# Optimization experiments

Measured on AMD Instinct MI355X. Metric: run time of the kernel, lower is better.

The kernel has to match this reference:

```python
import jax, jax.numpy as jnp
import numpy as np


def setup_inputs() -> dict:
    key = jax.random.key(0)
    k1, k2, k3, k4 = jax.random.split(key, 4)
    B, S, IN, H = 4, 2048, 512, 1024
    x = jax.random.normal(k1, (B, S, IN), dtype=jnp.float32)
    W1 = jax.random.normal(k2, (IN, H), dtype=jnp.float32) * (1.0 / np.sqrt(IN))
    b1 = jax.random.normal(k3, (H,), dtype=jnp.float32) * 0.02
    Wq = jax.random.normal(k4, (H, H), dtype=jnp.float32) * (1.0 / np.sqrt(H))
    return {"x": x, "W1": W1, "b1": b1, "Wq": Wq, "atten_size": 16}


def reference(x, W1, b1, Wq, atten_size):
    A = atten_size
    B, S, _ = x.shape
    H = W1.shape[1]
    h = jax.nn.relu(jnp.einsum('bsi,ih->bsh', x, W1) + b1)  # [B,S,H]
    # zero-pad sequence dim by A on each side
    padded = jnp.pad(h, ((0, 0), (A, A), (0, 0)))  # [B,S+2A,H]
    # torch: stack(roll(padded, k, 1) for k in -A..A, dim=2) then slice [A:-A]
    # => x_nei[b, i, j] = padded[b, 2A + i - j]
    idx = 2 * A + jnp.arange(S)[:, None] - jnp.arange(2 * A + 1)[None, :]  # [S,W]
    x_nei = padded[:, idx, :]  # [B,S,W,H]
    q = jnp.einsum('bsh,hk->bsk', h, Wq)  # [B,S,H]
    scores = jnp.einsum('bsh,bswh->bsw', q, x_nei) / jnp.sqrt(jnp.asarray(H, x.dtype))
    w = jax.nn.softmax(scores, axis=2)  # softmax over window axis
    out = jnp.einsum('bsw,bswh->bsh', w, x_nei)
    return out
```

## Files before the change

### kernel.cpp

```cpp
#include <hip/hip_runtime.h>
#include <stdint.h>

constexpr int BATCH = 4;
constexpr int SEQ   = 2048;
constexpr int DIN   = 512;
constexpr int DH    = 1024;
constexpr int BS    = BATCH * SEQ;
constexpr int AP    = 32;
constexpr int AW    = 64;

typedef float  floatx4 __attribute__((ext_vector_type(4)));
typedef short  bf16x8  __attribute__((ext_vector_type(8)));

static __device__ __forceinline__ unsigned short f2bf(float f) {
  union { float f; unsigned u; } v; v.f = f;
  unsigned r = (v.u + 0x7fffu + ((v.u >> 16) & 1u)) >> 16;
  return (unsigned short)r;
}

static __device__ __forceinline__ void gld_lds16(const unsigned short* g, const short* l) {
  typedef const __attribute__((address_space(1))) void* gvp;
  typedef __attribute__((address_space(3))) void* lvp;
  __builtin_amdgcn_global_load_lds((gvp)(uintptr_t)g, (lvp)(unsigned)(uintptr_t)l, 16, 0, 0);
}

__global__ __launch_bounds__(256) void prep_k(const float* __restrict__ X,
                                              const float* __restrict__ W1,
                                              const float* __restrict__ Wq,
                                              unsigned short* __restrict__ Xb,
                                              unsigned short* __restrict__ w1t,
                                              unsigned short* __restrict__ wqt) {
  __shared__ float t[32][33];
  if (blockIdx.y >= 48) {
    const int t0 = ((blockIdx.y - 48) * 32 + blockIdx.x) * 256 + threadIdx.x;
    const float4 a = ((const float4*)X)[(size_t)t0 * 2];
    const float4 b = ((const float4*)X)[(size_t)t0 * 2 + 1];
    __align__(16) unsigned short o[8];
    o[0] = f2bf(a.x); o[1] = f2bf(a.y); o[2] = f2bf(a.z); o[3] = f2bf(a.w);
    o[4] = f2bf(b.x); o[5] = f2bf(b.y); o[6] = f2bf(b.z); o[7] = f2bf(b.w);
    *(uint4*)(Xb + (size_t)t0 * 8) = *(const uint4*)o;
    return;
  }
  const bool isW1 = blockIdx.y < 16;
  const float* in = isW1 ? W1 : Wq;
  unsigned short* out = isW1 ? w1t : wqt;
  const int R = isW1 ? DIN : DH;
  const int C = DH;
  const int r0 = (isW1 ? blockIdx.y : (blockIdx.y - 16)) * 32;
  const int c0 = blockIdx.x * 32;
  const int tx = threadIdx.x & 31, ty = threadIdx.x >> 5;
  for (int i = ty; i < 32; i += 8) t[i][tx] = in[(size_t)(r0 + i) * C + c0 + tx];
  __syncthreads();
  for (int i = ty; i < 32; i += 8) out[(size_t)(c0 + i) * R + r0 + tx] = f2bf(t[tx][i]);
}

__global__ __launch_bounds__(256) void gemm1_k(const unsigned short* __restrict__ Ab,
                                               const unsigned short* __restrict__ Bt,
                                               const float* __restrict__ bias,
                                               unsigned short* __restrict__ outB,
                                               unsigned short* __restrict__ outBT) {
  const int M = BS, N = DH, K = DIN;
  __shared__ __align__(16) short As0[128 * 32], As1[128 * 32];
  __shared__ __align__(16) short Bs0[128 * 32], Bs1[128 * 32];
  const int tid  = threadIdx.x;
  const int m0   = blockIdx.x * 128, n0 = blockIdx.y * 128;
  const int wv   = tid >> 6, lane = tid & 63;
  const int wm   = (wv >> 1) * 64, wn = (wv & 1) * 64;
  const int l16  = lane & 15, quad = lane >> 4;

  const int ra = lane >> 2, ca = (lane & 3) * 8;
  const unsigned short* gA = Ab + (size_t)(m0 + wv * 32 + ra) * K + ca;
  const unsigned short* gB = Bt + (size_t)(n0 + wv * 32 + ra) * K + ca;
  const short* lA0a = &As0[wv * 1024];
  const short* lA0b = &As0[wv * 1024 + 512];
  const short* lA1a = &As1[wv * 1024];
  const short* lA1b = &As1[wv * 1024 + 512];
  const short* lB0a = &Bs0[wv * 1024];
  const short* lB0b = &Bs0[wv * 1024 + 512];
  const short* lB1a = &Bs1[wv * 1024];
  const short* lB1b = &Bs1[wv * 1024 + 512];

  floatx4 acc[4][4];
  for (int i = 0; i < 4; i++)
    for (int j = 0; j < 4; j++) acc[i][j] = {0.f, 0.f, 0.f, 0.f};

  for (int ks = 0; ks < K / 64; ++ks) {
    __syncthreads();
    gld_lds16(gA, lA0a); gld_lds16(gA + 16 * K, lA0b);
    gld_lds16(gA + 32, lA1a); gld_lds16(gA + 16 * K + 32, lA1b);
    gld_lds16(gB, lB0a); gld_lds16(gB + 16 * K, lB0b);
    gld_lds16(gB + 32, lB1a); gld_lds16(gB + 16 * K + 32, lB1b);
    gA += 64; gB += 64;
    __syncthreads();
    bf16x8 af[4], bfr[4];
    for (int i = 0; i < 4; i++)
      af[i] = *(const bf16x8*)&As0[(wm + i * 16 + l16) * 32 + quad * 8];
    for (int j = 0; j < 4; j++)
      bfr[j] = *(const bf16x8*)&Bs0[(wn + j * 16 + l16) * 32 + quad * 8];
    for (int i = 0; i < 4; i++)
      for (int j = 0; j < 4; j++)
        acc[i][j] = __builtin_amdgcn_mfma_f32_16x16x32_bf16(af[i], bfr[j], acc[i][j], 0, 0, 0);
    for (int i = 0; i < 4; i++)
      af[i] = *(const bf16x8*)&As1[(wm + i * 16 + l16) * 32 + quad * 8];
    for (int j = 0; j < 4; j++)
      bfr[j] = *(const bf16x8*)&Bs1[(wn + j * 16 + l16) * 32 + quad * 8];
    for (int i = 0; i < 4; i++)
      for (int j = 0; j < 4; j++)
        acc[i][j] = __builtin_amdgcn_mfma_f32_16x16x32_bf16(af[i], bfr[j], acc[i][j], 0, 0, 0);
  }

  for (int j = 0; j < 4; j++) {
    const int col = n0 + wn + j * 16 + l16;
    const float bv = bias[col];
    for (int i = 0; i < 4; i++) {
      const int rowb = m0 + wm + i * 16 + quad * 4;
      float v[4];
      for (int r = 0; r < 4; r++) v[r] = fmaxf(acc[i][j][r] + bv, 0.f);
      for (int r = 0; r < 4; r++) outB[(size_t)(rowb + r) * N + col] = f2bf(v[r]);
      ushort4 o4; o4.x = f2bf(v[0]); o4.y = f2bf(v[1]); o4.z = f2bf(v[2]); o4.w = f2bf(v[3]);
      *(ushort4*)(outBT + (size_t)col * M + rowb) = o4;
    }
  }
}

__global__ __launch_bounds__(1024, 4) void attn_fused_k(const unsigned short* __restrict__ hb,
                                                        const unsigned short* __restrict__ hbT,
                                                        const unsigned short* __restrict__ wqt,
                                                        float* __restrict__ out) {
  __shared__ __align__(16) unsigned short Hq[32 * 1024];
  __shared__ float Sf[2][32 * 64];
  __shared__ __align__(16) short Ps[32 * 72];

  const int tid  = threadIdx.x;
  const int wave = tid >> 6, lane = tid & 63;
  const int l16  = lane & 15, quad = lane >> 4;
  const int p0   = blockIdx.x * AP;
  const int s0   = p0 & (SEQ - 1);

  for (int i = tid; i < 32 * 72 / 2; i += 1024) ((unsigned*)Ps)[i] = 0;

  {
    const int r  = tid >> 5;
    const int c0 = (tid & 31) * 32;
    const unsigned short* src = hb + (size_t)(p0 + r) * DH + c0;
    #pragma unroll
    for (int c = 0; c < 4; c++) {
      uint4 v = *(const uint4*)(src + c * 8);
      const int colu = (c0 + c * 8) ^ ((r & 15) << 3);
      *(uint4*)&Hq[r * 1024 + colu] = v;
    }
  }
  __syncthreads();

  floatx4 qa[2][4];
  {
    for (int i = 0; i < 2; i++)
      for (int j = 0; j < 4; j++) qa[i][j] = {0.f, 0.f, 0.f, 0.f};
    const int wcol = wave * 64;
    const unsigned short* gq = wqt + (size_t)(wcol + l16) * DH + quad * 8;
    #pragma unroll 2
    for (int it = 0; it < 32; ++it) {
      const int cb = it * 32 + quad * 8;
      const int sw = cb ^ (l16 << 3);
      bf16x8 a0 = *(const bf16x8*)&Hq[l16 * 1024 + sw];
      bf16x8 a1 = *(const bf16x8*)&Hq[(16 + l16) * 1024 + sw];
      #pragma unroll
      for (int j = 0; j < 4; j++) {
        bf16x8 b = *(const bf16x8*)(gq + (size_t)(j * 16) * DH + it * 32);
        qa[0][j] = __builtin_amdgcn_mfma_f32_16x16x32_bf16(a0, b, qa[0][j], 0, 0, 0);
        qa[1][j] = __builtin_amdgcn_mfma_f32_16x16x32_bf16(a1, b, qa[1][j], 0, 0, 0);
      }
    }
  }
  __syncthreads();

  {
    const int wcol = wave * 64;
    for (int i = 0; i < 2; i++)
      for (int j = 0; j < 4; j++)
        for (int r = 0; r < 4; r++) {
          const int row  = i * 16 + quad * 4 + r;
          const int colu = wcol + j * 16 + l16;
          Hq[row * 1024 + (colu ^ ((row & 15) << 3))] = f2bf(qa[i][j][r]);
        }
  }
  __syncthreads();

  {
    const int kh = wave & 1;
    const int nt = (wave >> 1) & 3;
    const int mt = wave >> 3;
    const int qrow = mt * 16 + l16;
    const int hrow = s0 - 16 + nt * 16 + l16;
    const bool hv = (hrow >= 0) && (hrow < SEQ);
    const unsigned short* hp = hb + (long long)(p0 - 16 + nt * 16 + l16) * DH + kh * 512 + quad * 8;

    floatx4 ac[4] = {{0,0,0,0},{0,0,0,0},{0,0,0,0},{0,0,0,0}};
    const bf16x8 hz = {0,0,0,0,0,0,0,0};
    __builtin_amdgcn_s_setprio(1);
    #pragma unroll
    for (int it = 0; it < 16; ++it) {
      const int cb = kh * 512 + it * 32 + quad * 8;
      bf16x8 qf = *(const bf16x8*)&Hq[qrow * 1024 + (cb ^ (l16 << 3))];
      bf16x8 ha = hz;
      if (hv) ha = *(const bf16x8*)(hp + it * 32);
      ac[it & 3] = __builtin_amdgcn_mfma_f32_16x16x32_bf16(qf, ha, ac[it & 3], 0, 0, 0);
    }
    __builtin_amdgcn_s_setprio(0);
    floatx4 s4;
    for (int r = 0; r < 4; r++)
      s4[r] = (ac[0][r] + ac[1][r]) + (ac[2][r] + ac[3][r]);
    for (int r = 0; r < 4; r++)
      Sf[kh][(mt * 16 + quad * 4 + r) * 64 + nt * 16 + l16] = s4[r] * (1.f / 32.f);
  }
  __syncthreads();

  if (tid < 512) {
    const int row = tid >> 4, k = tid & 15;
    const float v0 = Sf[0][row * 64 + row + k] + Sf[1][row * 64 + row + k];
    const float v1 = Sf[0][row * 64 + row + k + 16] + Sf[1][row * 64 + row + k + 16];
    const float v2 = (k == 0) ? (Sf[0][row * 64 + row + 32] + Sf[1][row * 64 + row + 32]) : -1e30f;
    float mx = fmaxf(v0, fmaxf(v1, v2));
    for (int off = 1; off < 16; off <<= 1) mx = fmaxf(mx, __shfl_xor(mx, off, 64));
    const float e0 = __expf(v0 - mx), e1 = __expf(v1 - mx);
    const float e2 = (k == 0) ? __expf(v2 - mx) : 0.f;
    float sum = e0 + e1 + e2;
    for (int off = 1; off < 16; off <<= 1) sum += __shfl_xor(sum, off, 64);
    const float inv = 1.f / sum;
    Ps[row * 72 + row + k] = f2bf(e0 * inv);
    Ps[row * 72 + row + k + 16] = f2bf(e1 * inv);
    if (k == 0) Ps[row * 72 + row + 32] = f2bf(e2 * inv);
  }
  __syncthreads();

  {
    const bf16x8 pb00 = *(const bf16x8*)&Ps[(l16) * 72 + quad * 8];
    const bf16x8 pb01 = *(const bf16x8*)&Ps[(l16) * 72 + 32 + quad * 8];
    const bf16x8 pb10 = *(const bf16x8*)&Ps[(16 + l16) * 72 + quad * 8];
    const bf16x8 pb11 = *(const bf16x8*)&Ps[(16 + l16) * 72 + 32 + quad * 8];

    int lo = 16 - s0; if (lo < 0) lo = 0;
    int hi = SEQ + 16 - s0; if (hi > AW) hi = AW;
    const bool interior = (lo == 0) && (hi == AW);

    #pragma unroll
    for (int i = 0; i < 4; ++i) {
      const int mt2 = wave * 4 + i;
      const unsigned short* ap = hbT + (size_t)(mt2 * 16 + l16) * BS + (p0 - 16) + quad * 8;
      bf16x8 aa0 = *(const bf16x8*)(ap);
      bf16x8 aa1 = *(const bf16x8*)(ap + 32);
      if (!interior) {
        #pragma unroll
        for (int j = 0; j < 8; j++) {
          const int k = quad * 8 + j;
          if (k < lo || k >= hi) aa0[j] = 0;
          if (k + 32 < lo || k + 32 >= hi) aa1[j] = 0;
        }
      }
      floatx4 o0 = {0.f, 0.f, 0.f, 0.f}, o1 = {0.f, 0.f, 0.f, 0.f};
      __builtin_amdgcn_s_setprio(1);
      o0 = __builtin_amdgcn_mfma_f32_16x16x32_bf16(aa0, pb00, o0, 0, 0, 0);
      o0 = __builtin_amdgcn_mfma_f32_16x16x32_bf16(aa1, pb01, o0, 0, 0, 0);
      o1 = __builtin_amdgcn_mfma_f32_16x16x32_bf16(aa0, pb10, o1, 0, 0, 0);
      o1 = __builtin_amdgcn_mfma_f32_16x16x32_bf16(aa1, pb11, o1, 0, 0, 0);
      __builtin_amdgcn_s_setprio(0);
      float4 s0v; s0v.x = o0[0]; s0v.y = o0[1]; s0v.z = o0[2]; s0v.w = o0[3];
      float4 s1v; s1v.x = o1[0]; s1v.y = o1[1]; s1v.z = o1[2]; s1v.w = o1[3];
      *(float4*)(out + (size_t)(p0 + l16) * DH + mt2 * 16 + quad * 4) = s0v;
      *(float4*)(out + (size_t)(p0 + 16 + l16) * DH + mt2 * 16 + quad * 4) = s1v;
    }
  }
}

extern "C" void kernel_launch(void* const* d_in, const int* in_sizes, int n_in,
                              void* d_out, int out_size, void* d_ws, size_t ws_size,
                              hipStream_t stream) {
  const float* x  = (const float*)d_in[0];
  const float* W1 = (const float*)d_in[1];
  const float* b1 = (const float*)d_in[2];
  const float* Wq = (const float*)d_in[3];

  char* w = (char*)d_ws;
  unsigned short* w1t = (unsigned short*)(w);
  unsigned short* wqt = (unsigned short*)(w + (1ull  << 20));
  unsigned short* hb  = (unsigned short*)(w + (3ull  << 20));
  unsigned short* hbT = (unsigned short*)(w + (19ull << 20));
  unsigned short* xb  = (unsigned short*)(w + (35ull << 20));

  prep_k<<<dim3(32, 112), 256, 0, stream>>>(x, W1, Wq, xb, w1t, wqt);

  gemm1_k<<<dim3(BS / 128, DH / 128), 256, 0, stream>>>(xb, w1t, b1, hb, hbT);

  attn_fused_k<<<BS / AP, 1024, 0, stream>>>(hb, hbT, wqt, (float*)d_out);
}
```

Measured before the change: 186.6 us.

## Merge prep, GEMM and attention into one cooperative persistent kernel

Replaces the three separate launches with a single cooperative kernel of 256 blocks of 1024 threads, separating the phases with grid-wide syncs. The in-attention Q projection becomes a separate grid-wide GEMM that writes q to global memory (reusing the xb buffer), and the GEMM tiles now use 16 waves with 32x32 per-wave tiles. The aim is to remove launch overhead and the redundant per-block Q recomputation. In exchange it adds grid barriers, gives each wave a smaller MFMA tile, and adds an extra global round-trip for q. Aliasing qb onto xb is safe only because xb is no longer read once gemm1 has finished.

```diff
diff --git a/kernel.cpp b/kernel.cpp
--- a/kernel.cpp
+++ b/kernel.cpp
@@ -1,5 +1,8 @@
 #include <hip/hip_runtime.h>
+#include <hip/hip_cooperative_groups.h>
 #include <stdint.h>
+
+namespace cg = cooperative_groups;
 
 constexpr int BATCH = 4;
 constexpr int SEQ   = 2048;
@@ -24,250 +27,215 @@
   __builtin_amdgcn_global_load_lds((gvp)(uintptr_t)g, (lvp)(unsigned)(uintptr_t)l, 16, 0, 0);
 }
 
-__global__ __launch_bounds__(256) void prep_k(const float* __restrict__ X,
-                                              const float* __restrict__ W1,
-                                              const float* __restrict__ Wq,
-                                              unsigned short* __restrict__ Xb,
-                                              unsigned short* __restrict__ w1t,
-                                              unsigned short* __restrict__ wqt) {
-  __shared__ float t[32][33];
-  if (blockIdx.y >= 48) {
-    const int t0 = ((blockIdx.y - 48) * 32 + blockIdx.x) * 256 + threadIdx.x;
-    const float4 a = ((const float4*)X)[(size_t)t0 * 2];
-    const float4 b = ((const float4*)X)[(size_t)t0 * 2 + 1];
-    __align__(16) unsigned short o[8];
-    o[0] = f2bf(a.x); o[1] = f2bf(a.y); o[2] = f2bf(a.z); o[3] = f2bf(a.w);
-    o[4] = f2bf(b.x); o[5] = f2bf(b.y); o[6] = f2bf(b.z); o[7] = f2bf(b.w);
-    *(uint4*)(Xb + (size_t)t0 * 8) = *(const uint4*)o;
-    return;
-  }
-  const bool isW1 = blockIdx.y < 16;
-  const float* in = isW1 ? W1 : Wq;
-  unsigned short* out = isW1 ? w1t : wqt;
-  const int R = isW1 ? DIN : DH;
-  const int C = DH;
-  const int r0 = (isW1 ? blockIdx.y : (blockIdx.y - 16)) * 32;
-  const int c0 = blockIdx.x * 32;
-  const int tx = threadIdx.x & 31, ty = threadIdx.x >> 5;
-  for (int i = ty; i < 32; i += 8) t[i][tx] = in[(size_t)(r0 + i) * C + c0 + tx];
-  __syncthreads();
-  for (int i = ty; i < 32; i += 8) out[(size_t)(c0 + i) * R + r0 + tx] = f2bf(t[tx][i]);
-}
-
-__global__ __launch_bounds__(256) void gemm1_k(const unsigned short* __restrict__ Ab,
-                                               const unsigned short* __restrict__ Bt,
-                                               const float* __restrict__ bias,
-                                               unsigned short* __restrict__ outB,
-                                               unsigned short* __restrict__ outBT) {
-  const int M = BS, N = DH, K = DIN;
-  __shared__ __align__(16) short As0[128 * 32], As1[128 * 32];
-  __shared__ __align__(16) short Bs0[128 * 32], Bs1[128 * 32];
-  const int tid  = threadIdx.x;
-  const int m0   = blockIdx.x * 128, n0 = blockIdx.y * 128;
-  const int wv   = tid >> 6, lane = tid & 63;
-  const int wm   = (wv >> 1) * 64, wn = (wv & 1) * 64;
-  const int l16  = lane & 15, quad = lane >> 4;
-
+static __device__ __forceinline__ void do_gemm(
+    const unsigned short* __restrict__ Ab, const unsigned short* __restrict__ Bt,
+    const float* __restrict__ bias, unsigned short* __restrict__ outB,
+    unsigned short* __restrict__ outBT, int M, int N, int K, int m0, int n0,
+    int tid, char* smemc) {
+  short (*Sm)[128 * 32] = (short (*)[128 * 32])smemc;
+  const int wv = tid >> 6, lane = tid & 63;
+  const int wm = (wv >> 2) * 32, wn = (wv & 3) * 32;
+  const int l16 = lane & 15, quad = lane >> 4;
   const int ra = lane >> 2, ca = (lane & 3) * 8;
-  const unsigned short* gA = Ab + (size_t)(m0 + wv * 32 + ra) * K + ca;
-  const unsigned short* gB = Bt + (size_t)(n0 + wv * 32 + ra) * K + ca;
-  const short* lA0a = &As0[wv * 1024];
-  const short* lA0b = &As0[wv * 1024 + 512];
-  const short* lA1a = &As1[wv * 1024];
-  const short* lA1b = &As1[wv * 1024 + 512];
-  const short* lB0a = &Bs0[wv * 1024];
-  const short* lB0b = &Bs0[wv * 1024 + 512];
-  const short* lB1a = &Bs1[wv * 1024];
-  const short* lB1b = &Bs1[wv * 1024 + 512];
-
-  floatx4 acc[4][4];
-  for (int i = 0; i < 4; i++)
-    for (int j = 0; j < 4; j++) acc[i][j] = {0.f, 0.f, 0.f, 0.f};
+  const int wA = wv & 7;
+  const bool isB = wv >= 8;
+  const unsigned short* gS =
+      (isB ? Bt + (size_t)(n0 + wA * 16 + ra) * K : Ab + (size_t)(m0 + wA * 16 + ra) * K) + ca;
+  const short* l0 = &Sm[isB ? 2 : 0][wA * 512];
+  const short* l1 = &Sm[isB ? 3 : 1][wA * 512];
+
+  floatx4 acc[2][2];
+  for (int i = 0; i < 2; i++)
+    for (int j = 0; j < 2; j++) acc[i][j] = {0.f, 0.f, 0.f, 0.f};
 
   for (int ks = 0; ks < K / 64; ++ks) {
     __syncthreads();
-    gld_lds16(gA, lA0a); gld_lds16(gA + 16 * K, lA0b);
-    gld_lds16(gA + 32, lA1a); gld_lds16(gA + 16 * K + 32, lA1b);
-    gld_lds16(gB, lB0a); gld_lds16(gB + 16 * K, lB0b);
-    gld_lds16(gB + 32, lB1a); gld_lds16(gB + 16 * K + 32, lB1b);
-    gA += 64; gB += 64;
-    __syncthreads();
-    bf16x8 af[4], bfr[4];
-    for (int i = 0; i < 4; i++)
-      af[i] = *(const bf16x8*)&As0[(wm + i * 16 + l16) * 32 + quad * 8];
-    for (int j = 0; j < 4; j++)
-      bfr[j] = *(const bf16x8*)&Bs0[(wn + j * 16 + l16) * 32 + quad * 8];
-    for (int i = 0; i < 4; i++)
-      for (int j = 0; j < 4; j++)
-        acc[i][j] = __builtin_amdgcn_mfma_f32_16x16x32_bf16(af[i], bfr[j], acc[i][j], 0, 0, 0);
-    for (int i = 0; i < 4; i++)
-      af[i] = *(const bf16x8*)&As1[(wm + i * 16 + l16) * 32 + quad * 8];
-    for (int j = 0; j < 4; j++)
-      bfr[j] = *(const bf16x8*)&Bs1[(wn + j * 16 + l16) * 32 + quad * 8];
-    for (int i = 0; i < 4; i++)
-      for (int j = 0; j < 4; j++)
-        acc[i][j] = __builtin_amdgcn_mfma_f32_16x16x32_bf16(af[i], bfr[j], acc[i][j], 0, 0, 0);
-  }
-
-  for (int j = 0; j < 4; j++) {
+    gld_lds16(gS, l0);
+    gld_lds16(gS + 32, l1);
+    gS += 64;
+    __syncthreads();
+    bf16x8 a0 = *(const bf16x8*)&Sm[0][(wm + l16) * 32 + quad * 8];
+    bf16x8 a1 = *(const bf16x8*)&Sm[0][(wm + 16 + l16) * 32 + quad * 8];
+    bf16x8 b0 = *(const bf16x8*)&Sm[2][(wn + l16) * 32 + quad * 8];
+    bf16x8 b1 = *(const bf16x8*)&Sm[2][(wn + 16 + l16) * 32 + quad * 8];
+    acc[0][0] = __builtin_amdgcn_mfma_f32_16x16x32_bf16(a0, b0, acc[0][0], 0, 0, 0);
+    acc[0][1] = __builtin_amdgcn_mfma_f32_16x16x32_bf16(a0, b1, acc[0][1], 0, 0, 0);
+    acc[1][0] = __builtin_amdgcn_mfma_f32_16x16x32_bf16(a1, b0, acc[1][0], 0, 0, 0);
+    acc[1][1] = __builtin_amdgcn_mfma_f32_16x16x32_bf16(a1, b1, acc[1][1], 0, 0, 0);
+    a0 = *(const bf16x8*)&Sm[1][(wm + l16) * 32 + quad * 8];
+    a1 = *(const bf16x8*)&Sm[1][(wm + 16 + l16) * 32 + quad * 8];
+    b0 = *(const bf16x8*)&Sm[3][(wn + l16) * 32 + quad * 8];
+    b1 = *(const bf16x8*)&Sm[3][(wn + 16 + l16) * 32 + quad * 8];
+    acc[0][0] = __builtin_amdgcn_mfma_f32_16x16x32_bf16(a0, b0, acc[0][0], 0, 0, 0);
+    acc[0][1] = __builtin_amdgcn_mfma_f32_16x16x32_bf16(a0, b1, acc[0][1], 0, 0, 0);
+    acc[1][0] = __builtin_amdgcn_mfma_f32_16x16x32_bf16(a1, b0, acc[1][0], 0, 0, 0);
+    acc[1][1] = __builtin_amdgcn_mfma_f32_16x16x32_bf16(a1, b1, acc[1][1], 0, 0, 0);
+  }
+
+  for (int j = 0; j < 2; j++) {
     const int col = n0 + wn + j * 16 + l16;
-    const float bv = bias[col];
-    for (int i = 0; i < 4; i++) {
+    const float bv = bias ? bias[col] : 0.f;
+    for (int i = 0; i < 2; i++) {
       const int rowb = m0 + wm + i * 16 + quad * 4;
       float v[4];
-      for (int r = 0; r < 4; r++) v[r] = fmaxf(acc[i][j][r] + bv, 0.f);
+      for (int r = 0; r < 4; r++) {
+        float t = acc[i][j][r] + bv;
+        v[r] = bias ? fmaxf(t, 0.f) : t;
+      }
       for (int r = 0; r < 4; r++) outB[(size_t)(rowb + r) * N + col] = f2bf(v[r]);
-      ushort4 o4; o4.x = f2bf(v[0]); o4.y = f2bf(v[1]); o4.z = f2bf(v[2]); o4.w = f2bf(v[3]);
-      *(ushort4*)(outBT + (size_t)col * M + rowb) = o4;
-    }
-  }
-}
-
-__global__ __launch_bounds__(1024, 4) void attn_fused_k(const unsigned short* __restrict__ hb,
-                                                        const unsigned short* __restrict__ hbT,
-                                                        const unsigned short* __restrict__ wqt,
-                                                        float* __restrict__ out) {
-  __shared__ __align__(16) unsigned short Hq[32 * 1024];
-  __shared__ float Sf[2][32 * 64];
-  __shared__ __align__(16) short Ps[32 * 72];
-
-  const int tid  = threadIdx.x;
-  const int wave = tid >> 6, lane = tid & 63;
-  const int l16  = lane & 15, quad = lane >> 4;
-  const int p0   = blockIdx.x * AP;
-  const int s0   = p0 & (SEQ - 1);
-
-  for (int i = tid; i < 32 * 72 / 2; i += 1024) ((unsigned*)Ps)[i] = 0;
+      if (outBT) {
+        ushort4 o4;
+        o4.x = f2bf(v[0]); o4.y = f2bf(v[1]); o4.z = f2bf(v[2]); o4.w = f2bf(v[3]);
+        *(ushort4*)(outBT + (size_t)col * M + rowb) = o4;
+      }
+    }
+  }
+}
+
+__global__ __launch_bounds__(1024, 4) void mega_k(
+    const float* X, const float* W1g, const float* b1v, const float* Wqg,
+    unsigned short* xb, unsigned short* w1t, unsigned short* wqt,
+    unsigned short* hb, unsigned short* hbT, unsigned short* qb, float* out) {
+  __shared__ __align__(16) char smem[32768];
+  const int tid = threadIdx.x;
+  const int bid = blockIdx.x;
+  cg::grid_group grid = cg::this_grid();
 
   {
-    const int r  = tid >> 5;
-    const int c0 = (tid & 31) * 32;
-    const unsigned short* src = hb + (size_t)(p0 + r) * DH + c0;
+    const int gtid = bid * 1024 + tid;
     #pragma unroll
-    for (int c = 0; c < 4; c++) {
-      uint4 v = *(const uint4*)(src + c * 8);
-      const int colu = (c0 + c * 8) ^ ((r & 15) << 3);
-      *(uint4*)&Hq[r * 1024 + colu] = v;
-    }
-  }
-  __syncthreads();
-
-  floatx4 qa[2][4];
+    for (int k = 0; k < 2; k++) {
+      const size_t t0 = (size_t)gtid + (size_t)k * 262144;
+      const float4 a = ((const float4*)X)[t0 * 2];
+      const float4 b = ((const float4*)X)[t0 * 2 + 1];
+      __align__(16) unsigned short o[8];
+      o[0] = f2bf(a.x); o[1] = f2bf(a.y); o[2] = f2bf(a.z); o[3] = f2bf(a.w);
+      o[4] = f2bf(b.x); o[5] = f2bf(b.y); o[6] = f2bf(b.z); o[7] = f2bf(b.w);
+      *(uint4*)(xb + t0 * 8) = *(const uint4*)o;
+    }
+    float (*tt)[33] = (float (*)[33])(smem + (tid >> 8) * 4224);
+    const int stid = tid & 255;
+    const int tx = stid & 31, ty = stid >> 5;
+    for (int t = bid * 4 + (tid >> 8); t < 1536; t += 1024) {
+      const int by = t >> 5, bx = t & 31;
+      const bool isW1 = by < 16;
+      const float* in = isW1 ? W1g : Wqg;
+      unsigned short* ow = isW1 ? w1t : wqt;
+      const int R = isW1 ? DIN : DH;
+      const int r0 = (isW1 ? by : by - 16) * 32;
+      const int c0 = bx * 32;
+      __syncthreads();
+      for (int i = ty; i < 32; i += 8) tt[i][tx] = in[(size_t)(r0 + i) * DH + c0 + tx];
+      __syncthreads();
+      for (int i = ty; i < 32; i += 8) ow[(size_t)(c0 + i) * R + r0 + tx] = f2bf(tt[tx][i]);
+    }
+  }
+  __threadfence();
+  grid.sync();
+
+  for (int t = bid; t < 512; t += 256)
+    do_gemm(xb, w1t, b1v, hb, hbT, BS, DH, DIN, (t & 63) * 128, (t >> 6) * 128, tid, smem);
+  __threadfence();
+  grid.sync();
+
+  for (int t = bid; t < 512; t += 256)
+    do_gemm(hb, wqt, nullptr, qb, nullptr, BS, DH, DH, (t & 63) * 128, (t >> 6) * 128, tid, smem);
+  __threadfence();
+  grid.sync();
+
   {
-    for (int i = 0; i < 2; i++)
-      for (int j = 0; j < 4; j++) qa[i][j] = {0.f, 0.f, 0.f, 0.f};
-    const int wcol = wave * 64;
-    const unsigned short* gq = wqt + (size_t)(wcol + l16) * DH + quad * 8;
-    #pragma unroll 2
-    for (int it = 0; it < 32; ++it) {
-      const int cb = it * 32 + quad * 8;
-      const int sw = cb ^ (l16 << 3);
-      bf16x8 a0 = *(const bf16x8*)&Hq[l16 * 1024 + sw];
-      bf16x8 a1 = *(const bf16x8*)&Hq[(16 + l16) * 1024 + sw];
+    float* Sf = (float*)smem;
+    short* Ps = (short*)(smem + 16384);
+    const int wave = tid >> 6, lane = tid & 63;
+    const int l16 = lane & 15, quad = lane >> 4;
+    const int p0 = bid * AP;
+    const int s0 = p0 & (SEQ - 1);
+
+    for (int i = tid; i < 1152; i += 1024) ((unsigned*)(smem + 16384))[i] = 0;
+
+    {
+      const int kh = wave & 1;
+      const int nt = (wave >> 1) & 3;
+      const int mt = wave >> 3;
+      const unsigned short* qp = qb + (size_t)(p0 + mt * 16 + l16) * DH + kh * 512 + quad * 8;
+      const int hrow = s0 - 16 + nt * 16 + l16;
+      const bool hv = (hrow >= 0) && (hrow < SEQ);
+      const unsigned short* hp =
+          hb + (long long)(p0 - 16 + nt * 16 + l16) * DH + kh * 512 + quad * 8;
+
+      floatx4 ac[4] = {{0,0,0,0},{0,0,0,0},{0,0,0,0},{0,0,0,0}};
+      const bf16x8 hz = {0,0,0,0,0,0,0,0};
+      __builtin_amdgcn_s_setprio(1);
       #pragma unroll
-      for (int j = 0; j < 4; j++) {
-        bf16x8 b = *(const bf16x8*)(gq + (size_t)(j * 16) * DH + it * 32);
-        qa[0][j] = __builtin_amdgcn_mfma_f32_16x16x32_bf16(a0, b, qa[0][j], 0, 0, 0);
-        qa[1][j] = __builtin_amdgcn_mfma_f32_16x16x32_bf16(a1, b, qa[1][j], 0, 0, 0);
-      }
-    }
-  }
-  __syncthreads();
-
-  {
-    const int wcol = wave * 64;
-    for (int i = 0; i < 2; i++)
-      for (int j = 0; j < 4; j++)
-        for (int r = 0; r < 4; r++) {
-          const int row  = i * 16 + quad * 4 + r;
-          const int colu = wcol + j * 16 + l16;
-          Hq[row * 1024 + (colu ^ ((row & 15) << 3))] = f2bf(qa[i][j][r]);
+      for (int it = 0; it < 16; ++it) {
+        bf16x8 qa = *(const bf16x8*)(qp + it * 32);
+        bf16x8 ha = hz;
+        if (hv) ha = *(const bf16x8*)(hp + it * 32);
+        ac[it & 3] = __builtin_amdgcn_mfma_f32_16x16x32_bf16(qa, ha, ac[it & 3], 0, 0, 0);
+      }
+      __builtin_amdgcn_s_setprio(0);
+      floatx4 s4;
+      for (int r = 0; r < 4; r++) s4[r] = (ac[0][r] + ac[1][r]) + (ac[2][r] + ac[3][r]);
+      for (int r = 0; r < 4; r++)
+        Sf[kh * 2048 + (mt * 16 + quad * 4 + r) * 64 + nt * 16 + l16] = s4[r] * (1.f / 32.f);
+    }
+    __syncthreads();
+
+    if (tid < 512) {
+      const int row = tid >> 4, k = tid & 15;
+      const float v0 = Sf[row * 64 + row + k] + Sf[2048 + row * 64 + row + k];
+      const float v1 = Sf[row * 64 + row + k + 16] + Sf[2048 + row * 64 + row + k + 16];
+      const float v2 = (k == 0) ? (Sf[row * 64 + row + 32] + Sf[2048 + row * 64 + row + 32])
+                                : -1e30f;
+      float mx = fmaxf(v0, fmaxf(v1, v2));
+      for (int off = 1; off < 16; off <<= 1) mx = fmaxf(mx, __shfl_xor(mx, off, 64));
+      const float e0 = __expf(v0 - mx), e1 = __expf(v1 - mx);
+      const float e2 = (k == 0) ? __expf(v2 - mx) : 0.f;
+      float sum = e0 + e1 + e2;
+      for (int off = 1; off < 16; off <<= 1) sum += __shfl_xor(sum, off, 64);
+      const float inv = 1.f / sum;
+      Ps[row * 72 + row + k] = f2bf(e0 * inv);
+      Ps[row * 72 + row + k + 16] = f2bf(e1 * inv);
+      if (k == 0) Ps[row * 72 + row + 32] = f2bf(e2 * inv);
+    }
+    __syncthreads();
+
+    {
+      const bf16x8 pb00 = *(const bf16x8*)&Ps[(l16) * 72 + quad * 8];
+      const bf16x8 pb01 = *(const bf16x8*)&Ps[(l16) * 72 + 32 + quad * 8];
+      const bf16x8 pb10 = *(const bf16x8*)&Ps[(16 + l16) * 72 + quad * 8];
+      const bf16x8 pb11 = *(const bf16x8*)&Ps[(16 + l16) * 72 + 32 + quad * 8];
+
+      int lo = 16 - s0; if (lo < 0) lo = 0;
+      int hi = SEQ + 16 - s0; if (hi > AW) hi = AW;
+      const bool interior = (lo == 0) && (hi == AW);
+
+      #pragma unroll
+      for (int i = 0; i < 4; ++i) {
+        const int mt2 = wave * 4 + i;
+        const unsigned short* ap = hbT + (size_t)(mt2 * 16 + l16) * BS + (p0 - 16) + quad * 8;
+        bf16x8 aa0 = *(const bf16x8*)(ap);
+        bf16x8 aa1 = *(const bf16x8*)(ap + 32);
+        if (!interior) {
+          #pragma unroll
+          for (int j = 0; j < 8; j++) {
+            const int k = quad * 8 + j;
+            if (k < lo || k >= hi) aa0[j] = 0;
+            if (k + 32 < lo || k + 32 >= hi) aa1[j] = 0;
+          }
         }
-  }
-  __syncthreads();
-
-  {
-    const int kh = wave & 1;
-    const int nt = (wave >> 1) & 3;
-    const int mt = wave >> 3;
-    const int qrow = mt * 16 + l16;
-    const int hrow = s0 - 16 + nt * 16 + l16;
-    const bool hv = (hrow >= 0) && (hrow < SEQ);
-    const unsigned short* hp = hb + (long long)(p0 - 16 + nt * 16 + l16) * DH + kh * 512 + quad * 8;
-
-    floatx4 ac[4] = {{0,0,0,0},{0,0,0,0},{0,0,0,0},{0,0,0,0}};
-    const bf16x8 hz = {0,0,0,0,0,0,0,0};
-    __builtin_amdgcn_s_setprio(1);
-    #pragma unroll
-    for (int it = 0; it < 16; ++it) {
-      const int cb = kh * 512 + it * 32 + quad * 8;
-      bf16x8 qf = *(const bf16x8*)&Hq[qrow * 1024 + (cb ^ (l16 << 3))];
-      bf16x8 ha = hz;
-      if (hv) ha = *(const bf16x8*)(hp + it * 32);
-      ac[it & 3] = __builtin_amdgcn_mfma_f32_16x16x32_bf16(qf, ha, ac[it & 3], 0, 0, 0);
-    }
-    __builtin_amdgcn_s_setprio(0);
-    floatx4 s4;
-    for (int r = 0; r < 4; r++)
-      s4[r] = (ac[0][r] + ac[1][r]) + (ac[2][r] + ac[3][r]);
-    for (int r = 0; r < 4; r++)
-      Sf[kh][(mt * 16 + quad * 4 + r) * 64 + nt * 16 + l16] = s4[r] * (1.f / 32.f);
-  }
-  __syncthreads();
-
-  if (tid < 512) {
-    const int row = tid >> 4, k = tid & 15;
-    const float v0 = Sf[0][row * 64 + row + k] + Sf[1][row * 64 + row + k];
-    const float v1 = Sf[0][row * 64 + row + k + 16] + Sf[1][row * 64 + row + k + 16];
-    const float v2 = (k == 0) ? (Sf[0][row * 64 + row + 32] + Sf[1][row * 64 + row + 32]) : -1e30f;
-    float mx = fmaxf(v0, fmaxf(v1, v2));
-    for (int off = 1; off < 16; off <<= 1) mx = fmaxf(mx, __shfl_xor(mx, off, 64));
-    const float e0 = __expf(v0 - mx), e1 = __expf(v1 - mx);
-    const float e2 = (k == 0) ? __expf(v2 - mx) : 0.f;
-    float sum = e0 + e1 + e2;
-    for (int off = 1; off < 16; off <<= 1) sum += __shfl_xor(sum, off, 64);
-    const float inv = 1.f / sum;
-    Ps[row * 72 + row + k] = f2bf(e0 * inv);
-    Ps[row * 72 + row + k + 16] = f2bf(e1 * inv);
-    if (k == 0) Ps[row * 72 + row + 32] = f2bf(e2 * inv);
-  }
-  __syncthreads();
-
-  {
-    const bf16x8 pb00 = *(const bf16x8*)&Ps[(l16) * 72 + quad * 8];
-    const bf16x8 pb01 = *(const bf16x8*)&Ps[(l16) * 72 + 32 + quad * 8];
-    const bf16x8 pb10 = *(const bf16x8*)&Ps[(16 + l16) * 72 + quad * 8];
-    const bf16x8 pb11 = *(const bf16x8*)&Ps[(16 + l16) * 72 + 32 + quad * 8];
-
-    int lo = 16 - s0; if (lo < 0) lo = 0;
-    int hi = SEQ + 16 - s0; if (hi > AW) hi = AW;
-    const bool interior = (lo == 0) && (hi == AW);
-
-    #pragma unroll
-    for (int i = 0; i < 4; ++i) {
-      const int mt2 = wave * 4 + i;
-      const unsigned short* ap = hbT + (size_t)(mt2 * 16 + l16) * BS + (p0 - 16) + quad * 8;
-      bf16x8 aa0 = *(const bf16x8*)(ap);
-      bf16x8 aa1 = *(const bf16x8*)(ap + 32);
-      if (!interior) {
-        #pragma unroll
-        for (int j = 0; j < 8; j++) {
-          const int k = quad * 8 + j;
-          if (k < lo || k >= hi) aa0[j] = 0;
-          if (k + 32 < lo || k + 32 >= hi) aa1[j] = 0;
-        }
-      }
-      floatx4 o0 = {0.f, 0.f, 0.f, 0.f}, o1 = {0.f, 0.f, 0.f, 0.f};
-      __builtin_amdgcn_s_setprio(1);
-      o0 = __builtin_amdgcn_mfma_f32_16x16x32_bf16(aa0, pb00, o0, 0, 0, 0);
-      o0 = __builtin_amdgcn_mfma_f32_16x16x32_bf16(aa1, pb01, o0, 0, 0, 0);
-      o1 = __builtin_amdgcn_mfma_f32_16x16x32_bf16(aa0, pb10, o1, 0, 0, 0);
-      o1 = __builtin_amdgcn_mfma_f32_16x16x32_bf16(aa1, pb11, o1, 0, 0, 0);
-      __builtin_amdgcn_s_setprio(0);
-      float4 s0v; s0v.x = o0[0]; s0v.y = o0[1]; s0v.z = o0[2]; s0v.w = o0[3];
-      float4 s1v; s1v.x = o1[0]; s1v.y = o1[1]; s1v.z = o1[2]; s1v.w = o1[3];
-      *(float4*)(out + (size_t)(p0 + l16) * DH + mt2 * 16 + quad * 4) = s0v;
-      *(float4*)(out + (size_t)(p0 + 16 + l16) * DH + mt2 * 16 + quad * 4) = s1v;
+        floatx4 o0 = {0.f, 0.f, 0.f, 0.f}, o1 = {0.f, 0.f, 0.f, 0.f};
+        __builtin_amdgcn_s_setprio(1);
+        o0 = __builtin_amdgcn_mfma_f32_16x16x32_bf16(aa0, pb00, o0, 0, 0, 0);
+        o0 = __builtin_amdgcn_mfma_f32_16x16x32_bf16(aa1, pb01, o0, 0, 0, 0);
+        o1 = __builtin_amdgcn_mfma_f32_16x16x32_bf16(aa0, pb10, o1, 0, 0, 0);
+        o1 = __builtin_amdgcn_mfma_f32_16x16x32_bf16(aa1, pb11, o1, 0, 0, 0);
+        __builtin_amdgcn_s_setprio(0);
+        float4 s0v; s0v.x = o0[0]; s0v.y = o0[1]; s0v.z = o0[2]; s0v.w = o0[3];
+        float4 s1v; s1v.x = o1[0]; s1v.y = o1[1]; s1v.z = o1[2]; s1v.w = o1[3];
+        *(float4*)(out + (size_t)(p0 + l16) * DH + mt2 * 16 + quad * 4) = s0v;
+        *(float4*)(out + (size_t)(p0 + 16 + l16) * DH + mt2 * 16 + quad * 4) = s1v;
+      }
     }
   }
 }
@@ -285,11 +253,12 @@
   unsigned short* wqt = (unsigned short*)(w + (1ull  << 20));
   unsigned short* hb  = (unsigned short*)(w + (3ull  << 20));
   unsigned short* hbT = (unsigned short*)(w + (19ull << 20));
-  unsigned short* xb  = (unsigned short*)(w + (35ull << 20));
-
-  prep_k<<<dim3(32, 112), 256, 0, stream>>>(x, W1, Wq, xb, w1t, wqt);
-
-  gemm1_k<<<dim3(BS / 128, DH / 128), 256, 0, stream>>>(xb, w1t, b1, hb, hbT);
-
-  attn_fused_k<<<BS / AP, 1024, 0, stream>>>(hb, hbT, wqt, (float*)d_out);
-}
+  unsigned short* qb  = (unsigned short*)(w + (35ull << 20));
+  unsigned short* xb  = qb;
+  float* outp = (float*)d_out;
+
+  void* args[] = {(void*)&x,  (void*)&W1,  (void*)&b1,  (void*)&Wq,
+                  (void*)&xb, (void*)&w1t, (void*)&wqt,
+                  (void*)&hb, (void*)&hbT, (void*)&qb,  (void*)&outp};
+  hipLaunchCooperativeKernel(mega_k, dim3(256), dim3(1024), args, 0, stream);
+}
```

New measurement: 602.9 us. 223% more time.
